# Optimization experiments

Hardware: AMD Instinct MI355X
Metric: run time of the kernel (lower is better)

Reference implementation:

```python
import jax, jax.numpy as jnp
import numpy as np

N_PHENO = 50000
N_GENE = 50000
H = 128
N_LAYERS = 3  # num_layers=2 hidden convs + 1 final conv


def _seg_mean(x_src, edge, n_dst):
    # mean aggregation of source features onto destination nodes (PyG SAGEConv default)
    msg = x_src[edge[0]]                       # [E, H] gather
    s = jax.ops.segment_sum(msg, edge[1], num_segments=n_dst)
    cnt = jax.ops.segment_sum(jnp.ones((edge.shape[1],), x_src.dtype), edge[1], num_segments=n_dst)
    return s / jnp.maximum(cnt, 1.0)[:, None]


def _sage(x_src, x_dst, edge, Wl, bl, Wr, n_dst):
    # SAGEConv: lin_l(mean_j x_j) + lin_r(x_i); lin_l has bias, lin_r does not
    return _seg_mean(x_src, edge, n_dst) @ Wl + bl + x_dst @ Wr


def setup_inputs() -> dict:
    key = jax.random.key(0)
    ks = jax.random.split(key, 16)
    d = {
        'x_pheno': jax.random.normal(ks[0], (N_PHENO, H), jnp.float32),
        'x_gene': jax.random.normal(ks[1], (N_GENE, H), jnp.float32),
    }
    scale = 1.0 / np.sqrt(H)
    names = ['Wl_isa', 'bl_isa', 'Wr_isa', 'Wl_rel', 'bl_rel', 'Wr_rel', 'Wl_rev', 'bl_rev', 'Wr_rev']
    for i, nm in enumerate(names):
        shp = (N_LAYERS, H) if nm.startswith('b') else (N_LAYERS, H, H)
        d[nm] = jax.random.normal(ks[2 + i], shp, jnp.float32) * scale
    d['edge_isa'] = jax.random.randint(ks[11], (2, 500000), 0, N_PHENO, jnp.int64)
    d['edge_rel'] = jax.random.randint(ks[12], (2, 1000000), 0, N_GENE, jnp.int64)
    d['edge_rev'] = jax.random.randint(ks[13], (2, 1000000), 0, N_PHENO, jnp.int64)
    d['edge_label_index'] = jax.random.randint(ks[14], (2, 500000), 0, N_PHENO, jnp.int64)
    return d


def reference(x_pheno, x_gene, Wl_isa, bl_isa, Wr_isa, Wl_rel, bl_rel, Wr_rel,
              Wl_rev, bl_rev, Wr_rev, edge_isa, edge_rel, edge_rev, edge_label_index):
    xp, xg = x_pheno, x_gene
    n_p, n_g = xp.shape[0], xg.shape[0]
    for i in range(N_LAYERS):
        # HeteroConv aggr='sum': sum SAGE outputs across edge types per dst node type
        new_p = (_sage(xp, xp, edge_isa, Wl_isa[i], bl_isa[i], Wr_isa[i], n_p)
                 + _sage(xg, xp, edge_rev, Wl_rev[i], bl_rev[i], Wr_rev[i], n_p))
        new_g = _sage(xp, xg, edge_rel, Wl_rel[i], bl_rel[i], Wr_rel[i], n_g)
        if i < N_LAYERS - 1:  # leaky_relu after hidden convs, not after `final`
            new_p = jax.nn.leaky_relu(new_p, 0.01)
            new_g = jax.nn.leaky_relu(new_g, 0.01)
        xp, xg = new_p, new_g
    # Classifier: dot-product edge decoder + sigmoid
    score = (xp[edge_label_index[0]] * xg[edge_label_index[1]]).sum(axis=-1)
    return jax.nn.sigmoid(score)
```

## Files before the change

kernel.cpp:

```cpp
#include <hip/hip_runtime.h>
#include <hip/hip_bf16.h>
#include <math.h>

#define H 128
#define RS 136
#define BSH 9
#define BINW 512
#define BCAP 11264
#define BSLOT 12288
#define KEDGE 4096
#define EPT 16
#define MAXBINS 1024

typedef __attribute__((ext_vector_type(8))) short short8;
typedef __attribute__((ext_vector_type(4))) short short4v;
typedef __attribute__((ext_vector_type(2))) short short2v;
typedef __attribute__((ext_vector_type(4))) float f32x4;
typedef __attribute__((ext_vector_type(2))) _Float16 half2v;
typedef __attribute__((ext_vector_type(4))) _Float16 half4v;
typedef __attribute__((ext_vector_type(8))) _Float16 half8v;

__device__ __forceinline__ short f2bf(float f) {
    unsigned u = __float_as_uint(f);
    u += 0x7fff + ((u >> 16) & 1);
    return (short)(u >> 16);
}
__device__ __forceinline__ float bf2f(short h) {
    return __uint_as_float(((unsigned)(unsigned short)h) << 16);
}


__global__ __launch_bounds__(256) void bin_scatter_kernel(
    const int* __restrict__ e0, int E0, const int* __restrict__ e1, int E1,
    const int* __restrict__ e2, int E2, int* __restrict__ bin_cur,
    int* __restrict__ temp, int NPn, int NGn, int nbins, int E_tot) {
    __shared__ int hist[MAXBINS];
    __shared__ int cur[MAXBINS];
    int t = threadIdx.x;
    for (int i = t; i < nbins; i += 256) hist[i] = 0;
    __syncthreads();
    int vals[EPT], bins[EPT];
    int base_e = blockIdx.x * KEDGE;
#pragma unroll
    for (int j = 0; j < EPT; ++j) {
        int g = base_e + j * 256 + t;
        int b = -1, v = 0;
        if (g < E_tot) {
            const int* ed; int E, lo, nbase;
            if (g < E0) { ed = e0; E = E0; lo = g; nbase = 0; }
            else if (g < E0 + E1) { ed = e1; E = E1; lo = g - E0; nbase = NPn; }
            else { ed = e2; E = E2; lo = g - E0 - E1; nbase = NPn + NGn; }
            int src = ed[lo];
            int gdst = nbase + ed[E + lo];
            v = src | ((gdst & (BINW - 1)) << 16);
            b = gdst >> BSH;
            atomicAdd(&hist[b], 1);
        }
        vals[j] = v;
        bins[j] = b;
    }
    __syncthreads();
    for (int i = t; i < nbins; i += 256) {
        int h = hist[i];
        cur[i] = h ? atomicAdd(&bin_cur[i * 16], h) : 0;
    }
    __syncthreads();
#pragma unroll
    for (int j = 0; j < EPT; ++j) {
        if (bins[j] >= 0) {
            int p = atomicAdd(&cur[bins[j]], 1);
            if (p < BSLOT) temp[(size_t)bins[j] * BSLOT + p] = vals[j];
        }
    }
}

__global__ __launch_bounds__(1024) void scan_bins(const int* __restrict__ bin_cur, int nbins,
                                                  int* __restrict__ bin_base) {
    __shared__ int sh[1024];
    int t = threadIdx.x;
    int v = 0;
    if (t < nbins) { v = bin_cur[t * 16]; if (v > BSLOT) v = BSLOT; }
    sh[t] = v;
    __syncthreads();
    for (int off = 1; off < 1024; off <<= 1) {
        int u = (t >= off) ? sh[t - off] : 0;
        __syncthreads();
        sh[t] += u;
        __syncthreads();
    }
    if (t < nbins) bin_base[t] = sh[t] - v;
    if (t == nbins - 1) bin_base[nbins] = sh[t];
}

__global__ __launch_bounds__(256) void bin_sort_kernel(
    const int* __restrict__ bin_base, const int* __restrict__ temp,
    int* __restrict__ col, int* __restrict__ rowptr, int n_tot, int nbins) {
    __shared__ int srt[BCAP];
    __shared__ int cur[BINW];
    __shared__ int pfx[BINW];
    __shared__ int red[256];
    int b = blockIdx.x;
    int start = b << BSH;
    int nodes = n_tot - start; if (nodes > BINW) nodes = BINW;
    int t = threadIdx.x;
    int base = bin_base[b];
    int count = bin_base[b + 1] - base;
    const int* __restrict__ tb = temp + (size_t)b * BSLOT;
    for (int i = t; i < BINW; i += 256) cur[i] = 0;
    __syncthreads();
    for (int i = t; i < count; i += 256)
        atomicAdd(&cur[(tb[i] >> 16) & (BINW - 1)], 1);
    __syncthreads();
    int a0 = cur[2 * t], a1 = cur[2 * t + 1];
    red[t] = a0 + a1;
    __syncthreads();
    for (int off = 1; off < 256; off <<= 1) {
        int u = (t >= off) ? red[t - off] : 0;
        __syncthreads();
        red[t] += u;
        __syncthreads();
    }
    int excl = red[t] - (a0 + a1);
    pfx[2 * t] = excl;
    pfx[2 * t + 1] = excl + a0;
    __syncthreads();
    for (int i = t; i < nodes; i += 256) rowptr[start + i] = base + pfx[i];
    if (b == nbins - 1 && t == 0) rowptr[n_tot] = base + count;
    for (int i = t; i < BINW; i += 256) cur[i] = pfx[i];
    __syncthreads();
    if (count <= BCAP) {
        for (int i = t; i < count; i += 256) {
            int v = tb[i];
            int p = atomicAdd(&cur[(v >> 16) & (BINW - 1)], 1);
            srt[p] = v & 0xFFFF;
        }
        __syncthreads();
        for (int i = t; i < count; i += 256) col[base + i] = srt[i];
    } else {
        for (int i = t; i < count; i += 256) {
            int v = tb[i];
            int p = atomicAdd(&cur[(v >> 16) & (BINW - 1)], 1);
            col[base + p] = v & 0xFFFF;
        }
    }
}


struct WSrc { const float* a[15]; const float* b[15]; };

__global__ __launch_bounds__(256) void pack_w_kernel(WSrc src, short* __restrict__ whi,
                                                     short* __restrict__ wlo) {
    int idx = blockIdx.x * 256 + threadIdx.x;
    if (idx >= 15 * 4 * 8 * 64) return;
    int lane = idx & 63;
    int ct = (idx >> 6) & 7;
    int kc = (idx >> 9) & 3;
    int mat = idx >> 11;
    const float* A = src.a[mat];
    const float* Bp = src.b[mat];
    int n = ct * 16 + (lane & 15);
    int kbase = kc * 32 + (lane >> 4) * 8;
    size_t o = (size_t)idx * 8;
    for (int j = 0; j < 8; ++j) {
        float v = A[(size_t)(kbase + j) * H + n];
        if (Bp) v += Bp[(size_t)(kbase + j) * H + n];
        short h = f2bf(v);
        whi[o + j] = h;
        wlo[o + j] = f2bf(v - bf2f(h));
    }
}


__global__ __launch_bounds__(256) void cvt16_kernel(const float* __restrict__ xa, int n4a,
                                                    const float* __restrict__ xb, int n4b,
                                                    _Float16* __restrict__ ya,
                                                    _Float16* __restrict__ yb) {
    int i = blockIdx.x * 256 + threadIdx.x;
    const float* x; _Float16* y;
    if (i < n4a) { x = xa + (size_t)i * 4; y = ya + (size_t)i * 4; }
    else if (i < n4a + n4b) { x = xb + (size_t)(i - n4a) * 4; y = yb + (size_t)(i - n4a) * 4; }
    else return;
    f32x4 v = *(const f32x4*)x;
    half4v h;
#pragma unroll
    for (int k = 0; k < 4; ++k) h[k] = (_Float16)v[k];
    *(half4v*)y = h;
}


__device__ __forceinline__ void seg8x4(const _Float16* __restrict__ x,
                                       const int* __restrict__ rowptr,
                                       const int* __restrict__ col,
                                       const int rb[4], int voff, float2 out[4]) {
    int beg[4], cnt[4], last[4];
    int mc = 0;
#pragma unroll
    for (int r = 0; r < 4; ++r) {
        int b = rowptr[rb[r]];
        int e = rowptr[rb[r] + 1];
        int c = e - b;
        beg[r] = b;
        cnt[r] = c;
        last[r] = (c > 0) ? e - 1 : 0;
        int ch = (c + 7) >> 3;
        if (ch > mc) mc = ch;
    }
    float ax[4] = {0.f, 0.f, 0.f, 0.f};
    float ay[4] = {0.f, 0.f, 0.f, 0.f};
    for (int c = 0; c < mc; ++c) {
        half2v v[4][8];
#pragma unroll
        for (int r = 0; r < 4; ++r) {
            if (c * 8 < cnt[r]) {
#pragma unroll
                for (int i = 0; i < 8; ++i) {
                    int p = beg[r] + c * 8 + i;
                    if (p > last[r]) p = last[r];
                    int si = __builtin_amdgcn_readfirstlane(col[p]);
                    v[r][i] = *(const half2v*)(x + (size_t)si * H + voff);
                }
            }
        }
#pragma unroll
        for (int r = 0; r < 4; ++r) {
            if (c * 8 < cnt[r]) {
                int rem = cnt[r] - c * 8;
#pragma unroll
                for (int i = 0; i < 8; ++i) {
                    float m = (i < rem) ? 1.0f : 0.0f;
                    ax[r] = fmaf((float)v[r][i][0], m, ax[r]);
                    ay[r] = fmaf((float)v[r][i][1], m, ay[r]);
                }
            }
        }
    }
#pragma unroll
    for (int r = 0; r < 4; ++r) {
        int c = cnt[r]; if (c < 1) c = 1;
        float inv = 1.0f / (float)c;
        out[r] = (float2){ax[r] * inv, ay[r] * inv};
    }
}


struct GTerm {
    const _Float16* x;
    int rbase;
    const short* hi;
    const short* lo;
    const float* f;
};

template <int NIN>
__global__ __launch_bounds__(256, 3) void fused_gnn(
    GTerm t0, GTerm t1, GTerm t2,
    const int* __restrict__ rowptr, const int* __restrict__ col,
    const short* __restrict__ whi, const short* __restrict__ wlo,
    int mat0, int mat1, int mat2,
    const float* __restrict__ b0, const float* __restrict__ b1,
    _Float16* __restrict__ out16, short* __restrict__ ohi, short* __restrict__ olo,
    int n_rows, int relu) {
    __shared__ short Ahi[64 * RS];
    __shared__ short Alo[64 * RS];
    const int tid = threadIdx.x;
    const int lane = tid & 63;
    const int wave = __builtin_amdgcn_readfirstlane(tid >> 6);
    const int r0 = blockIdx.x * 64;
    const int ct0 = wave * 2;
    const int m16 = lane & 15;
    const int acol = (lane >> 4) * 8;

    f32x4 acc[4][2];
#pragma unroll
    for (int mt = 0; mt < 4; ++mt)
#pragma unroll
        for (int c = 0; c < 2; ++c) acc[mt][c] = (f32x4){0.f, 0.f, 0.f, 0.f};

    const GTerm terms[3] = {t0, t1, t2};
    const int marr[3] = {mat0, mat1, mat2};

#pragma unroll
    for (int m = 0; m < NIN; ++m) {
        const GTerm& T = terms[m];
        __syncthreads();
        if (T.x) {
            int voff = lane * 2;
#pragma unroll
            for (int g = 0; g < 4; ++g) {
                int rb[4];
#pragma unroll
                for (int r = 0; r < 4; ++r) {
                    int gr = r0 + wave * 16 + g * 4 + r;
                    if (gr >= n_rows) gr = n_rows - 1;
                    rb[r] = T.rbase + gr;
                }
                float2 s[4];
                seg8x4(T.x, rowptr, col, rb, voff, s);
#pragma unroll
                for (int r = 0; r < 4; ++r) {
                    int lrow = wave * 16 + g * 4 + r;
                    short h0 = f2bf(s[r].x), h1 = f2bf(s[r].y);
                    *(short2v*)&Ahi[lrow * RS + voff] = (short2v){h0, h1};
                    *(short2v*)&Alo[lrow * RS + voff] =
                        (short2v){f2bf(s[r].x - bf2f(h0)), f2bf(s[r].y - bf2f(h1))};
                }
            }
        } else if (T.hi) {
#pragma unroll
            for (int i = 0; i < 8; ++i) {
                int f = tid + i * 256;
                int row = f >> 5;
                int c4 = (f & 31) * 4;
                int gr = r0 + row;
                if (gr >= n_rows) gr = n_rows - 1;
                size_t o = (size_t)gr * H + c4;
                *(short4v*)&Ahi[row * RS + c4] = *(const short4v*)&T.hi[o];
                *(short4v*)&Alo[row * RS + c4] = *(const short4v*)&T.lo[o];
            }
        } else {
            const float* __restrict__ A = T.f;
#pragma unroll
            for (int i = 0; i < 8; ++i) {
                int f = tid + i * 256;
                int row = f >> 5;
                int c4 = (f & 31) * 4;
                int gr = r0 + row;
                if (gr >= n_rows) gr = n_rows - 1;
                float4 v = *(const float4*)&A[(size_t)gr * H + c4];
                short h0 = f2bf(v.x), h1 = f2bf(v.y), h2 = f2bf(v.z), h3 = f2bf(v.w);
                *(short4v*)&Ahi[row * RS + c4] = (short4v){h0, h1, h2, h3};
                *(short4v*)&Alo[row * RS + c4] =
                    (short4v){f2bf(v.x - bf2f(h0)), f2bf(v.y - bf2f(h1)),
                              f2bf(v.z - bf2f(h2)), f2bf(v.w - bf2f(h3))};
            }
        }
        __syncthreads();
        const short* __restrict__ wh = whi + (size_t)marr[m] * (H * H);
        const short* __restrict__ wl = wlo + (size_t)marr[m] * (H * H);
        short8 bh[2][2], bl[2][2];
        {
            size_t f0 = ((size_t)ct0 * 64 + lane) * 8;
            bh[0][0] = *(const short8*)&wh[f0];
            bh[0][1] = *(const short8*)&wh[f0 + 512];
            bl[0][0] = *(const short8*)&wl[f0];
            bl[0][1] = *(const short8*)&wl[f0 + 512];
        }
#pragma unroll
        for (int kc = 0; kc < 4; ++kc) {
            if (kc < 3) {
                int nb = (kc + 1) & 1;
                size_t f = ((size_t)((kc + 1) * 8 + ct0) * 64 + lane) * 8;
                bh[nb][0] = *(const short8*)&wh[f];
                bh[nb][1] = *(const short8*)&wh[f + 512];
                bl[nb][0] = *(const short8*)&wl[f];
                bl[nb][1] = *(const short8*)&wl[f + 512];
            }
            int cb = kc & 1;
#pragma unroll
            for (int mt = 0; mt < 4; ++mt) {
                short8 ah = *(const short8*)&Ahi[(mt * 16 + m16) * RS + kc * 32 + acol];
                short8 al = *(const short8*)&Alo[(mt * 16 + m16) * RS + kc * 32 + acol];
#pragma unroll
                for (int c = 0; c < 2; ++c) {
                    acc[mt][c] = __builtin_amdgcn_mfma_f32_16x16x32_bf16(ah, bh[cb][c], acc[mt][c], 0, 0, 0);
                    acc[mt][c] = __builtin_amdgcn_mfma_f32_16x16x32_bf16(al, bh[cb][c], acc[mt][c], 0, 0, 0);
                    acc[mt][c] = __builtin_amdgcn_mfma_f32_16x16x32_bf16(ah, bl[cb][c], acc[mt][c], 0, 0, 0);
                }
            }
        }
    }

    const int rquad = (lane >> 4) * 4;
    const int ncol = lane & 15;
#pragma unroll
    for (int c = 0; c < 2; ++c) {
        int n = (ct0 + c) * 16 + ncol;
        float bs = b0[n];
        if (b1) bs += b1[n];
#pragma unroll
        for (int mt = 0; mt < 4; ++mt) {
#pragma unroll
            for (int reg = 0; reg < 4; ++reg) {
                int gr = r0 + mt * 16 + rquad + reg;
                if (gr < n_rows) {
                    float v = acc[mt][c][reg] + bs;
                    if (relu) v = v > 0.f ? v : 0.01f * v;
                    size_t o = (size_t)gr * H + n;
                    out16[o] = (_Float16)v;
                    short h = f2bf(v);
                    ohi[o] = h;
                    olo[o] = f2bf(v - bf2f(h));
                }
            }
        }
    }
}


__global__ __launch_bounds__(256) void scores_kernel(const _Float16* __restrict__ xp,
                                                     const _Float16* __restrict__ xg,
                                                     const int* __restrict__ eli, int E,
                                                     float* __restrict__ out) {
    int lane16 = threadIdx.x & 15;
    int sub = threadIdx.x >> 4;
    int e = blockIdx.x * 16 + sub;
    if (e >= E) return;
    int ip = eli[e];
    int ig = eli[E + e];
    half8v a = *(const half8v*)&xp[(size_t)ip * H + lane16 * 8];
    half8v b = *(const half8v*)&xg[(size_t)ig * H + lane16 * 8];
    float s = 0.f;
#pragma unroll
    for (int k = 0; k < 8; ++k) s += (float)a[k] * (float)b[k];
#pragma unroll
    for (int off = 8; off; off >>= 1) s += __shfl_xor(s, off, 16);
    if (lane16 == 0) out[e] = 1.0f / (1.0f + expf(-s));
}


extern "C" void kernel_launch(void* const* d_in, const int* in_sizes, int n_in,
                              void* d_out, int out_size, void* d_ws, size_t ws_size,
                              hipStream_t stream) {
    const float* x_pheno = (const float*)d_in[0];
    const float* x_gene  = (const float*)d_in[1];
    const float* Wl_isa  = (const float*)d_in[2];
    const float* bl_isa  = (const float*)d_in[3];
    const float* Wr_isa  = (const float*)d_in[4];
    const float* Wl_rel  = (const float*)d_in[5];
    const float* bl_rel  = (const float*)d_in[6];
    const float* Wr_rel  = (const float*)d_in[7];
    const float* Wl_rev  = (const float*)d_in[8];
    const float* bl_rev  = (const float*)d_in[9];
    const float* Wr_rev  = (const float*)d_in[10];
    const int* e_isa = (const int*)d_in[11];
    const int* e_rel = (const int*)d_in[12];
    const int* e_rev = (const int*)d_in[13];
    const int* e_lbl = (const int*)d_in[14];
    const int E_isa = in_sizes[11] / 2;
    const int E_rel = in_sizes[12] / 2;
    const int E_rev = in_sizes[13] / 2;
    const int E_lbl = in_sizes[14] / 2;
    const int NP = in_sizes[0] / H;
    const int NG = in_sizes[1] / H;
    const int n_tot = NP + NG + NP;
    const int E_tot = E_isa + E_rel + E_rev;
    const int nbins = (n_tot + BINW - 1) / BINW;

    char* ws = (char*)d_ws;
    auto alloc = [&](size_t bytes) -> char* {
        char* p = ws;
        ws += (bytes + 255) & ~(size_t)255;
        return p;
    };
    int* rowptr  = (int*)alloc((size_t)(n_tot + 1) * 4);
    int* col     = (int*)alloc((size_t)E_tot * 4);
    int* temp    = (int*)alloc((size_t)nbins * BSLOT * 4);
    int* bin_cur = (int*)alloc((size_t)nbins * 16 * 4);
    int* bin_base= (int*)alloc((size_t)(nbins + 1) * 4);
    short* whi = (short*)alloc((size_t)15 * H * H * sizeof(short));
    short* wlo = (short*)alloc((size_t)15 * H * H * sizeof(short));
    _Float16* xpm[2], *xgm[2];
    xpm[0] = (_Float16*)alloc((size_t)NP * H * sizeof(_Float16));
    xpm[1] = (_Float16*)alloc((size_t)NP * H * sizeof(_Float16));
    xgm[0] = (_Float16*)alloc((size_t)NG * H * sizeof(_Float16));
    xgm[1] = (_Float16*)alloc((size_t)NG * H * sizeof(_Float16));
    short* xph = (short*)alloc((size_t)NP * H * sizeof(short));
    short* xpl = (short*)alloc((size_t)NP * H * sizeof(short));
    short* xgh = (short*)alloc((size_t)NG * H * sizeof(short));
    short* xgl = (short*)alloc((size_t)NG * H * sizeof(short));

    hipMemsetAsync(bin_cur, 0, (size_t)nbins * 16 * 4, stream);
    bin_scatter_kernel<<<(E_tot + KEDGE - 1) / KEDGE, 256, 0, stream>>>(
        e_isa, E_isa, e_rel, E_rel, e_rev, E_rev, bin_cur, temp, NP, NG, nbins, E_tot);
    scan_bins<<<1, 1024, 0, stream>>>(bin_cur, nbins, bin_base);
    bin_sort_kernel<<<nbins, 256, 0, stream>>>(bin_base, temp, col, rowptr, n_tot, nbins);

    WSrc src;
    for (int l = 0; l < 3; ++l) {
        src.a[l * 5 + 0] = Wl_isa + (size_t)l * H * H;  src.b[l * 5 + 0] = nullptr;
        src.a[l * 5 + 1] = Wl_rev + (size_t)l * H * H;  src.b[l * 5 + 1] = nullptr;
        src.a[l * 5 + 2] = Wr_isa + (size_t)l * H * H;  src.b[l * 5 + 2] = Wr_rev + (size_t)l * H * H;
        src.a[l * 5 + 3] = Wl_rel + (size_t)l * H * H;  src.b[l * 5 + 3] = nullptr;
        src.a[l * 5 + 4] = Wr_rel + (size_t)l * H * H;  src.b[l * 5 + 4] = nullptr;
    }
    pack_w_kernel<<<(15 * 4 * 8 * 64 + 255) / 256, 256, 0, stream>>>(src, whi, wlo);

    cvt16_kernel<<<((NP + NG) * 32 + 255) / 256, 256, 0, stream>>>(
        x_pheno, NP * 32, x_gene, NG * 32, xpm[0], xgm[0]);

    const short *pph = nullptr, *ppl = nullptr, *pgh = nullptr, *pgl = nullptr;
    for (int l = 0; l < 3; ++l) {
        int rs = l & 1;
        int wsid = rs ^ 1;
        int relu = (l < 2) ? 1 : 0;
        const float* bli = bl_isa + (size_t)l * H;
        const float* blv = bl_rev + (size_t)l * H;
        const float* blr = bl_rel + (size_t)l * H;
        GTerm isa{xpm[rs], 0, nullptr, nullptr, nullptr};
        GTerm rev{xgm[rs], NP + NG, nullptr, nullptr, nullptr};
        GTerm xpt{nullptr, 0, pph, ppl, l == 0 ? x_pheno : nullptr};
        fused_gnn<3><<<(NP + 63) / 64, 256, 0, stream>>>(
            isa, rev, xpt, rowptr, col, whi, wlo, l * 5 + 0, l * 5 + 1, l * 5 + 2,
            bli, blv, xpm[wsid], xph, xpl, NP, relu);
        GTerm rel{xpm[rs], NP, nullptr, nullptr, nullptr};
        GTerm xgt{nullptr, 0, pgh, pgl, l == 0 ? x_gene : nullptr};
        GTerm nil{nullptr, 0, nullptr, nullptr, nullptr};
        fused_gnn<2><<<(NG + 63) / 64, 256, 0, stream>>>(
            rel, xgt, nil, rowptr, col, whi, wlo, l * 5 + 3, l * 5 + 4, 0,
            blr, nullptr, xgm[wsid], xgh, xgl, NG, relu);
        pph = xph; ppl = xpl; pgh = xgh; pgl = xgl;
    }

    scores_kernel<<<(E_lbl + 15) / 16, 256, 0, stream>>>(xpm[1], xgm[1], e_lbl, E_lbl,
                                                         (float*)d_out);
}
```

Measured before the change: 686.3 us.

## Merge pheno and gene layer kernels into one launch; widen gather to 16 edges

The two per-layer fused GNN launches (pheno update and gene update) are merged into a single launch whose blocks branch on block index, so each layer becomes one larger grid. This removes a launch boundary and fills the tail of the pheno pass with gene work. The segment-mean gather now handles 2 rows with 16 edge loads in flight per row instead of 4 rows with 8 each, using split accumulators. The trade-off is higher register pressure from 32 outstanding index and value loads and from instantiating both template bodies in one kernel, which may reduce occupancy.

```diff
diff --git a/kernel.cpp b/kernel.cpp
--- a/kernel.cpp
+++ b/kernel.cpp
@@ -188,58 +188,54 @@
 }
 
 
-__device__ __forceinline__ void seg8x4(const _Float16* __restrict__ x,
-                                       const int* __restrict__ rowptr,
-                                       const int* __restrict__ col,
-                                       const int rb[4], int voff, float2 out[4]) {
-    int beg[4], cnt[4], last[4];
-    int mc = 0;
-#pragma unroll
-    for (int r = 0; r < 4; ++r) {
-        int b = rowptr[rb[r]];
-        int e = rowptr[rb[r] + 1];
-        int c = e - b;
-        beg[r] = b;
-        cnt[r] = c;
-        last[r] = (c > 0) ? e - 1 : 0;
-        int ch = (c + 7) >> 3;
-        if (ch > mc) mc = ch;
-    }
-    float ax[4] = {0.f, 0.f, 0.f, 0.f};
-    float ay[4] = {0.f, 0.f, 0.f, 0.f};
+__device__ __forceinline__ void seg16x2(const _Float16* __restrict__ x,
+                                        const int* __restrict__ rowptr,
+                                        const int* __restrict__ col,
+                                        int rb0, int rb1, int voff, float2 out[2]) {
+    int b0 = rowptr[rb0], e0 = rowptr[rb0 + 1];
+    int b1 = rowptr[rb1], e1 = rowptr[rb1 + 1];
+    int c0 = e0 - b0, c1 = e1 - b1;
+    int l0 = (c0 > 0) ? e0 - 1 : 0;
+    int l1 = (c1 > 0) ? e1 - 1 : 0;
+    int cmax = c0 > c1 ? c0 : c1;
+    int mc = (cmax + 15) >> 4;
+    float a0[4] = {0.f, 0.f, 0.f, 0.f}, y0[4] = {0.f, 0.f, 0.f, 0.f};
+    float a1[4] = {0.f, 0.f, 0.f, 0.f}, y1[4] = {0.f, 0.f, 0.f, 0.f};
     for (int c = 0; c < mc; ++c) {
-        half2v v[4][8];
-#pragma unroll
-        for (int r = 0; r < 4; ++r) {
-            if (c * 8 < cnt[r]) {
-#pragma unroll
-                for (int i = 0; i < 8; ++i) {
-                    int p = beg[r] + c * 8 + i;
-                    if (p > last[r]) p = last[r];
-                    int si = __builtin_amdgcn_readfirstlane(col[p]);
-                    v[r][i] = *(const half2v*)(x + (size_t)si * H + voff);
-                }
-            }
-        }
-#pragma unroll
-        for (int r = 0; r < 4; ++r) {
-            if (c * 8 < cnt[r]) {
-                int rem = cnt[r] - c * 8;
-#pragma unroll
-                for (int i = 0; i < 8; ++i) {
-                    float m = (i < rem) ? 1.0f : 0.0f;
-                    ax[r] = fmaf((float)v[r][i][0], m, ax[r]);
-                    ay[r] = fmaf((float)v[r][i][1], m, ay[r]);
-                }
-            }
-        }
-    }
-#pragma unroll
-    for (int r = 0; r < 4; ++r) {
-        int c = cnt[r]; if (c < 1) c = 1;
-        float inv = 1.0f / (float)c;
-        out[r] = (float2){ax[r] * inv, ay[r] * inv};
-    }
+        int s0[16], s1[16];
+#pragma unroll
+        for (int i = 0; i < 16; ++i) {
+            int p = b0 + c * 16 + i; if (p > l0) p = l0;
+            s0[i] = __builtin_amdgcn_readfirstlane(col[p]);
+        }
+#pragma unroll
+        for (int i = 0; i < 16; ++i) {
+            int p = b1 + c * 16 + i; if (p > l1) p = l1;
+            s1[i] = __builtin_amdgcn_readfirstlane(col[p]);
+        }
+        half2v v0[16], v1[16];
+#pragma unroll
+        for (int i = 0; i < 16; ++i) v0[i] = *(const half2v*)(x + (size_t)s0[i] * H + voff);
+#pragma unroll
+        for (int i = 0; i < 16; ++i) v1[i] = *(const half2v*)(x + (size_t)s1[i] * H + voff);
+        int r0 = c0 - c * 16;
+        int r1 = c1 - c * 16;
+#pragma unroll
+        for (int i = 0; i < 16; ++i) {
+            float m0 = (i < r0) ? 1.0f : 0.0f;
+            float m1 = (i < r1) ? 1.0f : 0.0f;
+            a0[i & 3] = fmaf((float)v0[i][0], m0, a0[i & 3]);
+            y0[i & 3] = fmaf((float)v0[i][1], m0, y0[i & 3]);
+            a1[i & 3] = fmaf((float)v1[i][0], m1, a1[i & 3]);
+            y1[i & 3] = fmaf((float)v1[i][1], m1, y1[i & 3]);
+        }
+    }
+    int d0 = c0 < 1 ? 1 : c0, d1 = c1 < 1 ? 1 : c1;
+    float i0 = 1.0f / (float)d0, i1 = 1.0f / (float)d1;
+    out[0] = (float2){((a0[0] + a0[1]) + (a0[2] + a0[3])) * i0,
+                      ((y0[0] + y0[1]) + (y0[2] + y0[3])) * i0};
+    out[1] = (float2){((a1[0] + a1[1]) + (a1[2] + a1[3])) * i1,
+                      ((y1[0] + y1[1]) + (y1[2] + y1[3])) * i1};
 }
 
 
@@ -252,20 +248,19 @@
 };
 
 template <int NIN>
-__global__ __launch_bounds__(256, 3) void fused_gnn(
+__device__ __forceinline__ void layer_body(
+    short* __restrict__ Ahi, short* __restrict__ Alo,
     GTerm t0, GTerm t1, GTerm t2,
     const int* __restrict__ rowptr, const int* __restrict__ col,
     const short* __restrict__ whi, const short* __restrict__ wlo,
     int mat0, int mat1, int mat2,
     const float* __restrict__ b0, const float* __restrict__ b1,
     _Float16* __restrict__ out16, short* __restrict__ ohi, short* __restrict__ olo,
-    int n_rows, int relu) {
-    __shared__ short Ahi[64 * RS];
-    __shared__ short Alo[64 * RS];
+    int n_rows, int relu, int bx) {
     const int tid = threadIdx.x;
     const int lane = tid & 63;
     const int wave = __builtin_amdgcn_readfirstlane(tid >> 6);
-    const int r0 = blockIdx.x * 64;
+    const int r0 = bx * 64;
     const int ct0 = wave * 2;
     const int m16 = lane & 15;
     const int acol = (lane >> 4) * 8;
@@ -286,19 +281,16 @@
         if (T.x) {
             int voff = lane * 2;
 #pragma unroll
-            for (int g = 0; g < 4; ++g) {
-                int rb[4];
-#pragma unroll
-                for (int r = 0; r < 4; ++r) {
-                    int gr = r0 + wave * 16 + g * 4 + r;
-                    if (gr >= n_rows) gr = n_rows - 1;
-                    rb[r] = T.rbase + gr;
-                }
-                float2 s[4];
-                seg8x4(T.x, rowptr, col, rb, voff, s);
-#pragma unroll
-                for (int r = 0; r < 4; ++r) {
-                    int lrow = wave * 16 + g * 4 + r;
+            for (int g = 0; g < 8; ++g) {
+                int gr0 = r0 + wave * 16 + g * 2;
+                int gr1 = gr0 + 1;
+                if (gr0 >= n_rows) gr0 = n_rows - 1;
+                if (gr1 >= n_rows) gr1 = n_rows - 1;
+                float2 s[2];
+                seg16x2(T.x, rowptr, col, T.rbase + gr0, T.rbase + gr1, voff, s);
+#pragma unroll
+                for (int r = 0; r < 2; ++r) {
+                    int lrow = wave * 16 + g * 2 + r;
                     short h0 = f2bf(s[r].x), h1 = f2bf(s[r].y);
                     *(short2v*)&Ahi[lrow * RS + voff] = (short2v){h0, h1};
                     *(short2v*)&Alo[lrow * RS + voff] =
@@ -393,6 +385,32 @@
                 }
             }
         }
+    }
+}
+
+struct LayerArgs {
+    GTerm p0, p1, p2, g0, g1;
+    const int* rowptr; const int* col;
+    const short* whi; const short* wlo;
+    int pm0, pm1, pm2, gm0, gm1;
+    const float* pb0; const float* pb1; const float* gb0;
+    _Float16* pout16; short* poh; short* pol; int np;
+    _Float16* gout16; short* goh; short* gol; int ng;
+    int relu; int nbp;
+};
+
+__global__ __launch_bounds__(256, 3) void fused_layer(LayerArgs a) {
+    __shared__ short Ahi[64 * RS];
+    __shared__ short Alo[64 * RS];
+    int bx = blockIdx.x;
+    if (bx < a.nbp) {
+        layer_body<3>(Ahi, Alo, a.p0, a.p1, a.p2, a.rowptr, a.col, a.whi, a.wlo,
+                      a.pm0, a.pm1, a.pm2, a.pb0, a.pb1,
+                      a.pout16, a.poh, a.pol, a.np, a.relu, bx);
+    } else {
+        layer_body<2>(Ahi, Alo, a.g0, a.g1, a.g1, a.rowptr, a.col, a.whi, a.wlo,
+                      a.gm0, a.gm1, 0, a.gb0, nullptr,
+                      a.gout16, a.goh, a.gol, a.ng, a.relu, bx - a.nbp);
     }
 }
 
@@ -489,25 +507,25 @@
         x_pheno, NP * 32, x_gene, NG * 32, xpm[0], xgm[0]);
 
     const short *pph = nullptr, *ppl = nullptr, *pgh = nullptr, *pgl = nullptr;
+    const int nbp = (NP + 63) / 64, nbg = (NG + 63) / 64;
     for (int l = 0; l < 3; ++l) {
         int rs = l & 1;
         int wsid = rs ^ 1;
-        int relu = (l < 2) ? 1 : 0;
-        const float* bli = bl_isa + (size_t)l * H;
-        const float* blv = bl_rev + (size_t)l * H;
-        const float* blr = bl_rel + (size_t)l * H;
-        GTerm isa{xpm[rs], 0, nullptr, nullptr, nullptr};
-        GTerm rev{xgm[rs], NP + NG, nullptr, nullptr, nullptr};
-        GTerm xpt{nullptr, 0, pph, ppl, l == 0 ? x_pheno : nullptr};
-        fused_gnn<3><<<(NP + 63) / 64, 256, 0, stream>>>(
-            isa, rev, xpt, rowptr, col, whi, wlo, l * 5 + 0, l * 5 + 1, l * 5 + 2,
-            bli, blv, xpm[wsid], xph, xpl, NP, relu);
-        GTerm rel{xpm[rs], NP, nullptr, nullptr, nullptr};
-        GTerm xgt{nullptr, 0, pgh, pgl, l == 0 ? x_gene : nullptr};
-        GTerm nil{nullptr, 0, nullptr, nullptr, nullptr};
-        fused_gnn<2><<<(NG + 63) / 64, 256, 0, stream>>>(
-            rel, xgt, nil, rowptr, col, whi, wlo, l * 5 + 3, l * 5 + 4, 0,
-            blr, nullptr, xgm[wsid], xgh, xgl, NG, relu);
+        LayerArgs a;
+        a.p0 = GTerm{xpm[rs], 0, nullptr, nullptr, nullptr};
+        a.p1 = GTerm{xgm[rs], NP + NG, nullptr, nullptr, nullptr};
+        a.p2 = GTerm{nullptr, 0, pph, ppl, l == 0 ? x_pheno : nullptr};
+        a.g0 = GTerm{xpm[rs], NP, nullptr, nullptr, nullptr};
+        a.g1 = GTerm{nullptr, 0, pgh, pgl, l == 0 ? x_gene : nullptr};
+        a.rowptr = rowptr; a.col = col; a.whi = whi; a.wlo = wlo;
+        a.pm0 = l * 5 + 0; a.pm1 = l * 5 + 1; a.pm2 = l * 5 + 2;
+        a.gm0 = l * 5 + 3; a.gm1 = l * 5 + 4;
+        a.pb0 = bl_isa + (size_t)l * H; a.pb1 = bl_rev + (size_t)l * H;
+        a.gb0 = bl_rel + (size_t)l * H;
+        a.pout16 = xpm[wsid]; a.poh = xph; a.pol = xpl; a.np = NP;
+        a.gout16 = xgm[wsid]; a.goh = xgh; a.gol = xgl; a.ng = NG;
+        a.relu = (l < 2) ? 1 : 0; a.nbp = nbp;
+        fused_layer<<<nbp + nbg, 256, 0, stream>>>(a);
         pph = xph; ppl = xpl; pgh = xgh; pgl = xgl;
     }
 
```

New measurement: 1.262 ms. +83.9%, slower.
